# Optimization experiments

Measured on AMD Instinct MI355X. Metric: run time of the kernel, lower is better.

Reference implementation:

```python
import jax, jax.numpy as jnp
import numpy as np
from jax import lax

# config (matches init_kwargs)
NUM_CLASSES = 10
SCORE_THRESH = 0.05
TOPK = 1000
DET_PER_IMG = 100
NMS_SCORE = 0.3
NMS_SIGMA = 0.5
IMG_H, IMG_W = 800.0, 1333.0
IOU_SUPPRESS = 0.8
BBOX_XFORM_CLIP = float(np.log(1000.0 / 16.0))
EPS = 1e-7


def setup_inputs() -> dict:
    key = jax.random.key(0)
    k1, k2, k3 = jax.random.split(key, 3)
    B, A, C = 8, 200000, NUM_CLASSES
    cls_logits = jax.random.normal(k1, (B, A, C), dtype=jnp.float32)
    bbox_regression = 0.5 * jax.random.normal(k2, (B, A, 4), dtype=jnp.float32)
    # plausible anchors: random centers + sizes inside the image, xyxy format
    u = jax.random.uniform(k3, (A, 6), dtype=jnp.float32)
    cx = u[:, 0] * IMG_W
    cy = u[:, 1] * IMG_H
    w = 16.0 + u[:, 2] * 200.0
    h = 16.0 + u[:, 3] * 200.0
    anchors = jnp.stack([cx - 0.5 * w, cy - 0.5 * h, cx + 0.5 * w, cy + 0.5 * h], axis=-1)
    return {"cls_logits": cls_logits, "bbox_regression": bbox_regression, "anchors": anchors}


def _decode(rel, anc):
    # torchvision BoxCoder.decode_single, weights (1,1,1,1). rel, anc: [K,4] xyxy anchors
    wa = anc[:, 2] - anc[:, 0]
    ha = anc[:, 3] - anc[:, 1]
    cxa = anc[:, 0] + 0.5 * wa
    cya = anc[:, 1] + 0.5 * ha
    dx, dy = rel[:, 0], rel[:, 1]
    dw = jnp.minimum(rel[:, 2], BBOX_XFORM_CLIP)
    dh = jnp.minimum(rel[:, 3], BBOX_XFORM_CLIP)
    cx = dx * wa + cxa
    cy = dy * ha + cya
    w = jnp.exp(dw) * wa
    h = jnp.exp(dh) * ha
    boxes = jnp.stack([cx - 0.5 * w, cy - 0.5 * h, cx + 0.5 * w, cy + 0.5 * h], axis=-1)
    # clip_boxes_to_image
    x = jnp.clip(boxes[:, 0::2], 0.0, IMG_W)
    y = jnp.clip(boxes[:, 1::2], 0.0, IMG_H)
    return jnp.stack([x[:, 0], y[:, 0], x[:, 1], y[:, 1]], axis=-1)


def _iou_one(box, boxes):
    # box [4] vs boxes [K,4] -> [K]
    lt = jnp.maximum(box[:2], boxes[:, :2])
    rb = jnp.minimum(box[2:], boxes[:, 2:])
    wh = jnp.clip(rb - lt, 0.0)
    inter = wh[:, 0] * wh[:, 1]
    a1 = (box[2] - box[0]) * (box[3] - box[1])
    a2 = (boxes[:, 2] - boxes[:, 0]) * (boxes[:, 3] - boxes[:, 1])
    return inter / (a1 + a2 - inter + EPS)


def _postprocess_one(logits, rel, anchors):
    # logits [A,C], rel [A,4], anchors [A,4]
    probs = jax.nn.sigmoid(logits)
    scores_all = jnp.max(probs, axis=-1)               # [A]
    labels_all = jnp.argmax(probs, axis=-1)            # [A]
    scores_all = jnp.where(scores_all > SCORE_THRESH, scores_all, 0.0)
    top_scores, top_idx = lax.top_k(scores_all, TOPK)  # [K]
    labels = labels_all[top_idx]
    boxes = _decode(rel[top_idx], anchors[top_idx])    # [K,4]

    K = TOPK
    # --- batched gaussian soft-NMS (same-label decay only) ---
    def soft_step(carry, _):
        sc, out = carry
        i = jnp.argmax(sc)
        s = sc[i]
        out = out.at[i].set(jnp.maximum(s, 0.0))
        ious = _iou_one(boxes[i], boxes)
        decay = jnp.where(labels == labels[i], jnp.exp(-(ious ** 2) / NMS_SIGMA), 1.0)
        sc = (sc * decay).at[i].set(-1.0)
        return (sc, out), None
    (_, decayed), _ = lax.scan(soft_step, (top_scores, jnp.zeros_like(top_scores)), None, length=K)
    keep = decayed > NMS_SCORE

    # --- sort by decayed score desc, greedy hard suppression at IoU>0.8 ---
    order = jnp.argsort(-decayed)
    b = boxes[order]
    s = decayed[order]
    l = labels[order]
    alive0 = keep[order]
    idxs = jnp.arange(K)

    def greedy_step(alive, i):
        ious = _iou_one(b[i], b)
        suppress = (ious > IOU_SUPPRESS) & (idxs > i)
        alive = jnp.where(alive[i], alive & ~suppress, alive)
        return alive, None
    alive, _ = lax.scan(greedy_step, alive0, idxs)

    final_scores = jnp.where(alive, s, -1.0)
    out_scores, out_i = lax.top_k(final_scores, DET_PER_IMG)  # preserves desc order of survivors
    return b[out_i], out_scores, l[out_i]


def reference(cls_logits, bbox_regression, anchors):
    boxes, scores, labels = jax.vmap(_postprocess_one, in_axes=(0, 0, None))(
        cls_logits, bbox_regression, anchors)
    return boxes, scores, labels  # [B,D,4], [B,D], [B,D] (score -1 = padding)
```

## Files before the change

kernel.cpp:

```cpp
#include <hip/hip_runtime.h>
#include <math.h>

#define NCLS 10
#define TOPK 1000
#define DETS 100
#define CANDMAX 4096
#define SLOTS 16
#define ACTK 256
#define TILE 256

#define NB2 256
#define MGATE (-2.9444389791664403f)
#define SEAM 2.2f
#define SCA 30.907200f
#define SCB 41.0f
#define NBLK 64

__device__ __forceinline__ float sigmoidf_(float x) {
    return 1.0f / (1.0f + expf(-x));
}

__device__ __forceinline__ int mbin_(float m) {
    if (!(m > MGATE)) return 0;
    int b;
    if (m > SEAM) { b = 161 + (int)((m - SEAM) * SCB); if (b > 255) b = 255; }
    else          { b = 1 + (int)((m - MGATE) * SCA);  if (b > 160) b = 160; }
    return b;
}

__device__ __forceinline__ float key_score(const unsigned long long* key, int c) {
    return __uint_as_float(~(unsigned)(key[c] >> 32));
}

__device__ __forceinline__ unsigned fkey_(float f) {
    unsigned b = __float_as_uint(f);
    return (b & 0x80000000u) ? ~b : (b | 0x80000000u);
}
__device__ __forceinline__ float funkey_(unsigned k) {
    return __uint_as_float((k & 0x80000000u) ? (k & 0x7FFFFFFFu) : ~k);
}

__device__ __forceinline__ unsigned wave_umax_(unsigned x) {
    unsigned t;
    t = (unsigned)__builtin_amdgcn_update_dpp(0, (int)x, 0x111, 0xF, 0xF, false); x = (x > t) ? x : t;
    t = (unsigned)__builtin_amdgcn_update_dpp(0, (int)x, 0x112, 0xF, 0xF, false); x = (x > t) ? x : t;
    t = (unsigned)__builtin_amdgcn_update_dpp(0, (int)x, 0x114, 0xF, 0xF, false); x = (x > t) ? x : t;
    t = (unsigned)__builtin_amdgcn_update_dpp(0, (int)x, 0x118, 0xF, 0xF, false); x = (x > t) ? x : t;
    t = (unsigned)__builtin_amdgcn_update_dpp(0, (int)x, 0x142, 0xF, 0xF, false); x = (x > t) ? x : t;
    t = (unsigned)__builtin_amdgcn_update_dpp(0, (int)x, 0x143, 0xF, 0xF, false); x = (x > t) ? x : t;
    return (unsigned)__builtin_amdgcn_readlane((int)x, 63);
}

__global__ __launch_bounds__(256) void k_score_bins(const float* __restrict__ logits,
                                                    unsigned char* __restrict__ binc,
                                                    unsigned* hist,
                                                    unsigned* __restrict__ done,
                                                    unsigned* __restrict__ P,
                                                    int A) {
    __shared__ float tilef[TILE * NCLS];
    __shared__ unsigned h[4][NB2];
    __shared__ int s_last;
    int img = blockIdx.y;
    int tid = threadIdx.x;
    for (int i = tid; i < 4 * NB2; i += 256) ((unsigned*)h)[i] = 0;
    __syncthreads();

    const float* base = logits + (size_t)img * A * NCLS;
    unsigned char* bc = binc + (size_t)img * A;
    int rep = tid & 3;

    int ntile = A / TILE;
    for (int tile = blockIdx.x; tile < ntile; tile += NBLK) {
        const float4* src = (const float4*)(base + (size_t)tile * TILE * NCLS);
        float4 v0 = src[tid];
        float4 v1 = src[256 + tid];
        float4 v2;
        if (tid < 128) v2 = src[512 + tid];
        ((float4*)tilef)[tid] = v0;
        ((float4*)tilef)[256 + tid] = v1;
        if (tid < 128) ((float4*)tilef)[512 + tid] = v2;
        __syncthreads();
        float m = tilef[tid * 10];
#pragma unroll
        for (int c = 1; c < 10; ++c) m = fmaxf(m, tilef[tid * 10 + c]);
        int b = mbin_(m);
        bc[(size_t)tile * TILE + tid] = (unsigned char)b;
        if (b) atomicAdd(&h[rep][b], 1u);
        __syncthreads();
    }
    if (blockIdx.x == 0) {
        for (int a = ntile * TILE + tid; a < A; a += 256) {
            const float* lp2 = base + (size_t)a * NCLS;
            float m = lp2[0];
            for (int c = 1; c < 10; ++c) m = fmaxf(m, lp2[c]);
            int b = mbin_(m);
            bc[a] = (unsigned char)b;
            if (b) atomicAdd(&h[rep][b], 1u);
        }
    }
    __syncthreads();
    for (int i = tid; i < NB2; i += 256) {
        unsigned c = h[0][i] + h[1][i] + h[2][i] + h[3][i];
        if (c) atomicAdd(&hist[(size_t)img * NB2 + i], c);
    }
    __syncthreads();
    if (tid == 0) {
        __threadfence();
        unsigned old = atomicAdd(&done[img], 1u);
        s_last = (old == (unsigned)(NBLK - 1)) ? 1 : 0;
    }
    __syncthreads();
    if (s_last && tid < 64) {
        int lane = tid;
        unsigned* hh = hist + (size_t)img * NB2;
        unsigned b4[4];
        unsigned s = 0;
#pragma unroll
        for (int j = 0; j < 4; ++j) { b4[j] = atomicAdd(&hh[lane * 4 + j], 0u); s += b4[j]; }
        unsigned suf = s;
#pragma unroll
        for (int d = 1; d < 64; d <<= 1) {
            unsigned o = __shfl_down(suf, d);
            if (lane + d < 64) suf += o;
        }
        unsigned above = __shfl_down(suf, 1);
        if (lane == 63) above = 0;
        if (lane == 0 && suf < (unsigned)TOPK) P[img] = 0u;
        if (above < (unsigned)TOPK && suf >= (unsigned)TOPK) {
            unsigned cum = above;
            for (int j = 3; j >= 0; --j) {
                cum += b4[j];
                if (cum >= (unsigned)TOPK) { P[img] = (unsigned)(lane * 4 + j); break; }
            }
        }
    }
}

__global__ __launch_bounds__(256) void k_compact(const float* __restrict__ logits,
                                                 const unsigned char* __restrict__ binc,
                                                 const unsigned* __restrict__ P,
                                                 unsigned* __restrict__ ctr,
                                                 unsigned long long* __restrict__ cand,
                                                 int A) {
    int img = blockIdx.y;
    unsigned p = P[img];
    unsigned psel = p ? (p - 1u) : 0u;
    int lane = threadIdx.x & 63;
    const float* base = logits + (size_t)img * A * NCLS;
    const unsigned* b4 = (const unsigned*)(binc + (size_t)img * A);
    int nquad = A >> 2;
    for (int q = blockIdx.x * 256 + threadIdx.x; q < nquad; q += NBLK * 256) {
        unsigned ub = b4[q];
#pragma unroll
        for (int j = 0; j < 4; ++j) {
            unsigned bj = (ub >> (8 * j)) & 0xFFu;
            bool take = (psel == 0u) || (bj >= psel);
            unsigned long long mask = __ballot(take);
            if (mask) {
                int cnt = __popcll(mask);
                int leader = __ffsll((unsigned long long)mask) - 1;
                unsigned pos = 0;
                if (lane == leader) pos = atomicAdd(&ctr[img], (unsigned)cnt);
                pos = (unsigned)__shfl((int)pos, leader);
                if (take) {
                    unsigned slot = pos + (unsigned)__popcll(mask & ((1ull << lane) - 1ull));
                    if (slot < CANDMAX) {
                        unsigned a = (unsigned)(q * 4 + j);
                        const float* lp = base + (size_t)a * NCLS;
                        float m = lp[0];
#pragma unroll
                        for (int c = 1; c < 10; ++c) m = fmaxf(m, lp[c]);
                        float sc = sigmoidf_(m);
                        sc = (sc > 0.05f) ? sc : 0.0f;
                        unsigned bits = __float_as_uint(sc);
                        cand[(size_t)img * CANDMAX + slot] =
                            ((unsigned long long)bits << 32) | (unsigned)(~a);
                    }
                }
            }
        }
    }
    int tail0 = nquad << 2;
    if (blockIdx.x == 0) {
        for (int a = tail0 + (int)threadIdx.x; a < A; a += 256) {
            unsigned bj = binc[(size_t)img * A + a];
            if ((psel == 0u) || (bj >= psel)) {
                const float* lp = base + (size_t)a * NCLS;
                float m = lp[0];
                for (int c = 1; c < 10; ++c) m = fmaxf(m, lp[c]);
                float sc = sigmoidf_(m);
                sc = (sc > 0.05f) ? sc : 0.0f;
                unsigned bits = __float_as_uint(sc);
                unsigned pos = atomicAdd(&ctr[img], 1u);
                if (pos < CANDMAX)
                    cand[(size_t)img * CANDMAX + pos] =
                        ((unsigned long long)bits << 32) | (unsigned)(~a);
            }
        }
    }
}

__global__ __launch_bounds__(1024) void k_sortnms(const unsigned long long* __restrict__ cand,
                                                  const unsigned* __restrict__ ctr,
                                                  const float* __restrict__ logits,
                                                  const float* __restrict__ rel,
                                                  const float* __restrict__ anch,
                                                  float* __restrict__ out, int A, int B) {
    __shared__ unsigned long long key[CANDMAX];
    __shared__ float s_box[TOPK][4];
    __shared__ int   s_lab[TOPK];
    __shared__ float s_pbox[TOPK][4];
    __shared__ int   s_plab[TOPK];
    __shared__ float s_psc[TOPK];
    __shared__ int   s_alive[TOPK];

    const float CLIPV = 4.135166556742356f;
    const float EPS = 1e-7f;
    const float W_ = 1333.0f, H_ = 800.0f;

    int img = blockIdx.x;
    int tid = threadIdx.x;

    unsigned n = ctr[img];
    if (n > CANDMAX) n = CANDMAX;
    int L = (n <= 1024) ? 1024 : (n <= 2048) ? 2048 : CANDMAX;
    for (int i = tid; i < L; i += 1024)
        key[i] = (i < (int)n) ? ~cand[(size_t)img * CANDMAX + i] : ~0ull;
    __syncthreads();
    for (int k = 2; k <= L; k <<= 1) {
        for (int j = k >> 1; j > 0; j >>= 1) {
            for (int i = tid; i < L; i += 1024) {
                int l = i ^ j;
                if (l > i) {
                    unsigned long long va = key[i], vb = key[l];
                    bool up = ((i & k) == 0);
                    if (up ? (va > vb) : (va < vb)) { key[i] = vb; key[l] = va; }
                }
            }
            __syncthreads();
        }
    }
    for (int i = L + tid; i < CANDMAX; i += 1024) key[i] = ~0ull;
    __syncthreads();

    if (tid < TOPK) {
        unsigned long long ik = key[tid];
        unsigned ai = (unsigned)ik;
        if (ai >= (unsigned)A) ai = 0;
        const float* lp = logits + ((size_t)img * A + ai) * NCLS;
        float best = sigmoidf_(lp[0]); int lbb = 0;
#pragma unroll
        for (int cc = 1; cc < NCLS; ++cc) {
            float v = sigmoidf_(lp[cc]);
            if (v > best) { best = v; lbb = cc; }
        }
        const float* rp = rel + ((size_t)img * A + ai) * 4;
        const float* ap = anch + (size_t)ai * 4;
        float a0 = ap[0], a1 = ap[1], a2 = ap[2], a3 = ap[3];
        float wa = a2 - a0, ha = a3 - a1;
        float cxa = a0 + 0.5f * wa, cya = a1 + 0.5f * ha;
        float dx = rp[0], dy = rp[1];
        float dw = fminf(rp[2], CLIPV), dh = fminf(rp[3], CLIPV);
        float cx = dx * wa + cxa, cy = dy * ha + cya;
        float w = expf(dw) * wa, h = expf(dh) * ha;
        s_box[tid][0] = fminf(fmaxf(cx - 0.5f * w, 0.0f), W_);
        s_box[tid][1] = fminf(fmaxf(cy - 0.5f * h, 0.0f), H_);
        s_box[tid][2] = fminf(fmaxf(cx + 0.5f * w, 0.0f), W_);
        s_box[tid][3] = fminf(fmaxf(cy + 0.5f * h, 0.0f), H_);
        s_lab[tid] = lbb;
    }
    __syncthreads();
    if (tid >= 64) return;
    int lane = tid;

    int M = TOPK;
    int need_full = 0;
    float bound = key_score(key, ACTK);

    {
        float sc[4], x1[4], y1[4], x2[4], y2[4], ar[4];
        int lb[4];
#pragma unroll
        for (int j = 0; j < 4; ++j) {
            int c = lane + (j << 6);
            float4 bb = *(const float4*)&s_box[c][0];
            x1[j] = bb.x; y1[j] = bb.y; x2[j] = bb.z; y2[j] = bb.w;
            ar[j] = (bb.z - bb.x) * (bb.w - bb.y);
            lb[j] = s_lab[c];
            sc[j] = key_score(key, c);
        }

        int nconf = 0, Mf = -1;

        for (int t = 0; t < ACTK; ++t) {
            float bv = sc[0]; int bj = 0;
#pragma unroll
            for (int j = 1; j < 4; ++j)
                if (sc[j] > bv) { bv = sc[j]; bj = j; }
            unsigned mk = fkey_(bv);
            unsigned mx = wave_umax_(mk);
            float pcur = funkey_(mx);

            if (!(pcur >= bound)) { need_full = 1; break; }

            int pick = -1;
#pragma unroll
            for (int jj = 0; jj < 4; ++jj) {
                if (pick < 0) {
                    unsigned long long mj = __ballot(mk == mx && bj == jj);
                    if (mj) pick = (jj << 6) + (__ffsll(mj) - 1);
                }
            }

            float psc = fmaxf(pcur, 0.0f);
            float4 pb = *(const float4*)&s_box[pick][0];
            int plab_ = s_lab[pick];
            if (lane == 0) {
                *(float4*)&s_pbox[t][0] = pb;
                s_plab[t] = plab_;
                s_psc[t] = psc;
            }

            float4 qb[4]; int ga[4];
#pragma unroll
            for (int k = 0; k < 4; ++k) {
                int p = lane + (k << 6);
                int pc2 = (p < t) ? p : 0;
                qb[k] = *(const float4*)&s_pbox[pc2][0];
                ga[k] = (p < t) ? s_alive[pc2] : 0;
            }

            float wax = (pb.z - pb.x) * (pb.w - pb.y);
#pragma unroll
            for (int j = 0; j < 4; ++j) {
                float lx2 = fmaxf(pb.x, x1[j]), ly2 = fmaxf(pb.y, y1[j]);
                float rx2 = fminf(pb.z, x2[j]), ry2 = fminf(pb.w, y2[j]);
                float iw2 = fmaxf(rx2 - lx2, 0.0f), ih2 = fmaxf(ry2 - ly2, 0.0f);
                float inter2 = iw2 * ih2;
                bool hot = (inter2 > 0.0f) && (lb[j] == plab_);
                if (__ballot(hot) != 0ull) {
                    float iou2 = inter2 / (wax + ar[j] - inter2 + EPS);
                    float ie = (lb[j] == plab_) ? iou2 : 0.0f;
                    sc[j] *= expf(-(ie * ie) / 0.5f);
                }
            }
#pragma unroll
            for (int j = 0; j < 4; ++j)
                if (lane + (j << 6) == pick) sc[j] = -1.0f;

            bool sup = false;
#pragma unroll
            for (int k = 0; k < 4; ++k) {
                if (ga[k]) {
                    float lx = fmaxf(pb.x, qb[k].x), ly = fmaxf(pb.y, qb[k].y);
                    float rx = fminf(pb.z, qb[k].z), ry = fminf(pb.w, qb[k].w);
                    float iw = fmaxf(rx - lx, 0.0f), ih = fmaxf(ry - ly, 0.0f);
                    float inter = iw * ih;
                    float qa = (qb[k].z - qb[k].x) * (qb[k].w - qb[k].y);
                    float iou = inter / (wax + qa - inter + EPS);
                    sup = sup || (iou > 0.8f);
                }
            }
            bool alive = (psc > 0.3f) && (__ballot(sup) == 0ull);
            if (lane == 0) s_alive[t] = alive ? 1 : 0;
            nconf += alive ? 1 : 0;
            if (nconf >= DETS) { Mf = t + 1; break; }
        }
        if (!need_full) {
            if (Mf < 0) need_full = 1;
            else M = Mf;
        }
    }

    if (need_full) {
        float sc[SLOTS], x1[SLOTS], y1[SLOTS], x2[SLOTS], y2[SLOTS], ar[SLOTS];
        int lb[SLOTS];
#pragma unroll
        for (int j = 0; j < SLOTS; ++j) {
            int c = lane + (j << 6);
            if (c < TOPK) {
                float4 bb = *(const float4*)&s_box[c][0];
                x1[j] = bb.x; y1[j] = bb.y; x2[j] = bb.z; y2[j] = bb.w;
                ar[j] = (bb.z - bb.x) * (bb.w - bb.y);
                lb[j] = s_lab[c];
                sc[j] = key_score(key, c);
            } else {
                sc[j] = -2.0f; lb[j] = -1;
                x1[j] = y1[j] = x2[j] = y2[j] = ar[j] = 0.0f;
            }
        }
        unsigned long long aw = 0;
        if (lane < 15) aw = ~0ull;
        else if (lane == 15) aw = (1ull << (TOPK - 15 * 64)) - 1;
        int f = 0, nconf = 0;
        M = TOPK;
        for (int t = 0; t < TOPK; ++t) {
            int fp = (f < TOPK) ? f : 0;
            float4 fb = *(const float4*)&s_box[fp][0];
            int flab = s_lab[fp];
            int fs = f >> 6;
            float v = sc[0];
#pragma unroll
            for (int j = 1; j < SLOTS; ++j) if (fs == j) v = sc[j];
            float cf = __shfl(v, f & 63);
            float lm = sc[0];
#pragma unroll
            for (int j = 1; j < SLOTS; ++j) lm = fmaxf(lm, sc[j]);
            int pick; float pcur; float4 pb; int plab_;
            unsigned long long bb2 = __ballot(lm > cf);
            if (bb2 == 0) {
                pick = f; pcur = cf; pb = fb; plab_ = flab;
            } else {
                float bv = sc[0]; int bi = lane;
#pragma unroll
                for (int j = 1; j < SLOTS; ++j) {
                    int e = lane + (j << 6);
                    if (sc[j] > bv) { bv = sc[j]; bi = e; }
                }
#pragma unroll
                for (int d = 32; d; d >>= 1) {
                    float ov = __shfl_xor(bv, d);
                    int oi = __shfl_xor(bi, d);
                    if (ov > bv || (ov == bv && oi < bi)) { bv = ov; bi = oi; }
                }
                pick = bi; pcur = bv;
                pb = *(const float4*)&s_box[pick][0];
                plab_ = s_lab[pick];
            }
            float psc = fmaxf(pcur, 0.0f);
            if (lane == 0) {
                *(float4*)&s_pbox[t][0] = pb;
                s_plab[t] = plab_;
                s_psc[t] = psc;
            }
            bool alive = (psc > 0.3f);
            if (alive && t > 0) {
                float pa = (pb.z - pb.x) * (pb.w - pb.y);
                int kprev = ((t - 1) >> 6) + 1;
                bool sup = false;
                for (int k = 0; k < kprev; ++k) {
                    int p = lane + (k << 6);
                    int pc = (p < t) ? p : 0;
                    float4 qb = *(const float4*)&s_pbox[pc][0];
                    int ga = s_alive[pc];
                    if (p < t && ga) {
                        float lx = fmaxf(pb.x, qb.x), ly = fmaxf(pb.y, qb.y);
                        float rx = fminf(pb.z, qb.z), ry = fminf(pb.w, qb.w);
                        float iw = fmaxf(rx - lx, 0.0f), ih = fmaxf(ry - ly, 0.0f);
                        float inter = iw * ih;
                        float qa = (qb.z - qb.x) * (qb.w - qb.y);
                        float iou = inter / (pa + qa - inter + EPS);
                        sup = sup || (iou > 0.8f);
                    }
                }
                alive = (__ballot(sup) == 0ull);
            }
            if (lane == 0) s_alive[t] = alive ? 1 : 0;
            nconf += alive ? 1 : 0;
            if (nconf >= DETS) { M = t + 1; break; }
            float wax = (pb.z - pb.x) * (pb.w - pb.y);
#pragma unroll
            for (int j = 0; j < SLOTS; ++j) {
                float lx2 = fmaxf(pb.x, x1[j]), ly2 = fmaxf(pb.y, y1[j]);
                float rx2 = fminf(pb.z, x2[j]), ry2 = fminf(pb.w, y2[j]);
                float iw2 = fmaxf(rx2 - lx2, 0.0f), ih2 = fmaxf(ry2 - ly2, 0.0f);
                float inter2 = iw2 * ih2;
                bool hot = (inter2 > 0.0f) && (lb[j] == plab_);
                if (__ballot(hot) != 0ull) {
                    float iou2 = inter2 / (wax + ar[j] - inter2 + EPS);
                    float ie = (lb[j] == plab_) ? iou2 : 0.0f;
                    sc[j] *= expf(-(ie * ie) / 0.5f);
                }
            }
#pragma unroll
            for (int j = 0; j < SLOTS; ++j)
                if (lane + (j << 6) == pick) sc[j] = -1.0f;
            if (lane == (pick >> 6)) aw &= ~(1ull << (pick & 63));
            if (pick == f) {
                int fw = f >> 6;
                unsigned long long w2 = __shfl(aw, fw);
                while (w2 == 0ull && fw < 15) { ++fw; w2 = __shfl(aw, fw); }
                f = (w2 == 0ull) ? TOPK : (fw << 6) + (__ffsll(w2) - 1);
            }
        }
    }

    float* out_boxes  = out;
    float* out_scores = out + (size_t)B * DETS * 4;
    float* out_labels = out + (size_t)B * DETS * 5;
    int kmax = (M + 63) >> 6;
    int base = 0;
    for (int k = 0; k < kmax; ++k) {
        int p = lane + (k << 6);
        bool av = (p < M) && (s_alive[p] != 0);
        unsigned long long mask = __ballot(av);
        int slot = base + (int)__popcll(mask & ((1ull << lane) - 1ull));
        if (av && slot < DETS) {
            float4 pb = *(const float4*)&s_pbox[p][0];
            float* ob = out_boxes + ((size_t)img * DETS + slot) * 4;
            ob[0] = pb.x; ob[1] = pb.y; ob[2] = pb.z; ob[3] = pb.w;
            out_scores[img * DETS + slot] = s_psc[p];
            out_labels[img * DETS + slot] = (float)s_plab[p];
        }
        base += (int)__popcll(mask);
    }
    if (base < DETS) {
        int dbase = 0;
        for (int k = 0; k < kmax; ++k) {
            int p = lane + (k << 6);
            bool dd = (p < M) && (s_alive[p] == 0);
            unsigned long long mask = __ballot(dd);
            int slot = base + dbase + (int)__popcll(mask & ((1ull << lane) - 1ull));
            if (dd && slot < DETS) {
                float4 pb = *(const float4*)&s_pbox[p][0];
                float* ob = out_boxes + ((size_t)img * DETS + slot) * 4;
                ob[0] = pb.x; ob[1] = pb.y; ob[2] = pb.z; ob[3] = pb.w;
                out_scores[img * DETS + slot] = -1.0f;
                out_labels[img * DETS + slot] = (float)s_plab[p];
            }
            dbase += (int)__popcll(mask);
        }
    }
}

extern "C" void kernel_launch(void* const* d_in, const int* in_sizes, int n_in,
                              void* d_out, int out_size, void* d_ws, size_t ws_size,
                              hipStream_t stream) {
    const float* logits = (const float*)d_in[0];
    const float* rel = (const float*)d_in[1];
    const float* anch = (const float*)d_in[2];
    float* out = (float*)d_out;

    int A = in_sizes[2] / 4;
    int B = in_sizes[0] / (A * NCLS);

    char* w = (char*)d_ws;
    unsigned* hist = (unsigned*)w;           w += (size_t)B * NB2 * 4;
    unsigned* ctr = (unsigned*)w;            w += (size_t)B * 4;
    unsigned* done = (unsigned*)w;           w += (size_t)B * 4;
    size_t zbytes = (size_t)(w - (char*)d_ws);
    unsigned long long* cand = (unsigned long long*)w; w += (size_t)B * CANDMAX * 8;
    unsigned* P = (unsigned*)w;              w += (size_t)B * 4;
    unsigned char* binc = (unsigned char*)w;

    hipMemsetAsync(d_ws, 0, zbytes, stream);

    dim3 g1(NBLK, (unsigned)B);
    k_score_bins<<<g1, 256, 0, stream>>>(logits, binc, hist, done, P, A);
    k_compact<<<g1, 256, 0, stream>>>(logits, binc, P, ctr, cand, A);
    k_sortnms<<<B, 1024, 0, stream>>>(cand, ctr, logits, rel, anch, out, A, B);
}
```

Measured before the change: 258.1 us.

## Fuse candidate compaction into sort kernel and widen histogram grid

```diff
diff --git a/kernel.cpp b/kernel.cpp
--- a/kernel.cpp
+++ b/kernel.cpp
@@ -14,7 +14,7 @@
 #define SEAM 2.2f
 #define SCA 30.907200f
 #define SCB 41.0f
-#define NBLK 64
+#define NBLKB 256
 
 __device__ __forceinline__ float sigmoidf_(float x) {
     return 1.0f / (1.0f + expf(-x));
@@ -70,7 +70,7 @@
     int rep = tid & 3;
 
     int ntile = A / TILE;
-    for (int tile = blockIdx.x; tile < ntile; tile += NBLK) {
+    for (int tile = blockIdx.x; tile < ntile; tile += NBLKB) {
         const float4* src = (const float4*)(base + (size_t)tile * TILE * NCLS);
         float4 v0 = src[tid];
         float4 v1 = src[256 + tid];
@@ -107,7 +107,7 @@
     if (tid == 0) {
         __threadfence();
         unsigned old = atomicAdd(&done[img], 1u);
-        s_last = (old == (unsigned)(NBLK - 1)) ? 1 : 0;
+        s_last = (old == (unsigned)(NBLKB - 1)) ? 1 : 0;
     }
     __syncthreads();
     if (s_last && tid < 64) {
@@ -136,72 +136,8 @@
     }
 }
 
-__global__ __launch_bounds__(256) void k_compact(const float* __restrict__ logits,
-                                                 const unsigned char* __restrict__ binc,
-                                                 const unsigned* __restrict__ P,
-                                                 unsigned* __restrict__ ctr,
-                                                 unsigned long long* __restrict__ cand,
-                                                 int A) {
-    int img = blockIdx.y;
-    unsigned p = P[img];
-    unsigned psel = p ? (p - 1u) : 0u;
-    int lane = threadIdx.x & 63;
-    const float* base = logits + (size_t)img * A * NCLS;
-    const unsigned* b4 = (const unsigned*)(binc + (size_t)img * A);
-    int nquad = A >> 2;
-    for (int q = blockIdx.x * 256 + threadIdx.x; q < nquad; q += NBLK * 256) {
-        unsigned ub = b4[q];
-#pragma unroll
-        for (int j = 0; j < 4; ++j) {
-            unsigned bj = (ub >> (8 * j)) & 0xFFu;
-            bool take = (psel == 0u) || (bj >= psel);
-            unsigned long long mask = __ballot(take);
-            if (mask) {
-                int cnt = __popcll(mask);
-                int leader = __ffsll((unsigned long long)mask) - 1;
-                unsigned pos = 0;
-                if (lane == leader) pos = atomicAdd(&ctr[img], (unsigned)cnt);
-                pos = (unsigned)__shfl((int)pos, leader);
-                if (take) {
-                    unsigned slot = pos + (unsigned)__popcll(mask & ((1ull << lane) - 1ull));
-                    if (slot < CANDMAX) {
-                        unsigned a = (unsigned)(q * 4 + j);
-                        const float* lp = base + (size_t)a * NCLS;
-                        float m = lp[0];
-#pragma unroll
-                        for (int c = 1; c < 10; ++c) m = fmaxf(m, lp[c]);
-                        float sc = sigmoidf_(m);
-                        sc = (sc > 0.05f) ? sc : 0.0f;
-                        unsigned bits = __float_as_uint(sc);
-                        cand[(size_t)img * CANDMAX + slot] =
-                            ((unsigned long long)bits << 32) | (unsigned)(~a);
-                    }
-                }
-            }
-        }
-    }
-    int tail0 = nquad << 2;
-    if (blockIdx.x == 0) {
-        for (int a = tail0 + (int)threadIdx.x; a < A; a += 256) {
-            unsigned bj = binc[(size_t)img * A + a];
-            if ((psel == 0u) || (bj >= psel)) {
-                const float* lp = base + (size_t)a * NCLS;
-                float m = lp[0];
-                for (int c = 1; c < 10; ++c) m = fmaxf(m, lp[c]);
-                float sc = sigmoidf_(m);
-                sc = (sc > 0.05f) ? sc : 0.0f;
-                unsigned bits = __float_as_uint(sc);
-                unsigned pos = atomicAdd(&ctr[img], 1u);
-                if (pos < CANDMAX)
-                    cand[(size_t)img * CANDMAX + pos] =
-                        ((unsigned long long)bits << 32) | (unsigned)(~a);
-            }
-        }
-    }
-}
-
-__global__ __launch_bounds__(1024) void k_sortnms(const unsigned long long* __restrict__ cand,
-                                                  const unsigned* __restrict__ ctr,
+__global__ __launch_bounds__(1024) void k_sortnms(const unsigned char* __restrict__ binc,
+                                                  const unsigned* __restrict__ P,
                                                   const float* __restrict__ logits,
                                                   const float* __restrict__ rel,
                                                   const float* __restrict__ anch,
@@ -213,6 +149,7 @@
     __shared__ int   s_plab[TOPK];
     __shared__ float s_psc[TOPK];
     __shared__ int   s_alive[TOPK];
+    __shared__ unsigned s_n;
 
     const float CLIPV = 4.135166556742356f;
     const float EPS = 1e-7f;
@@ -220,13 +157,73 @@
 
     int img = blockIdx.x;
     int tid = threadIdx.x;
-
-    unsigned n = ctr[img];
+    const float* base = logits + (size_t)img * A * NCLS;
+
+    if (tid == 0) s_n = 0;
+    __syncthreads();
+    {
+        unsigned p = P[img];
+        unsigned psel = p ? (p - 1u) : 0u;
+        const unsigned* b4 = (const unsigned*)(binc + (size_t)img * A);
+        int nquad = A >> 2;
+        int nq4 = nquad >> 2;
+        for (int g = tid; g < nq4; g += 1024) {
+            uint4 u = ((const uint4*)b4)[g];
+            unsigned ws[4] = {u.x, u.y, u.z, u.w};
+#pragma unroll
+            for (int w2 = 0; w2 < 4; ++w2) {
+                unsigned ub = ws[w2];
+#pragma unroll
+                for (int j = 0; j < 4; ++j) {
+                    unsigned bj = (ub >> (8 * j)) & 0xFFu;
+                    if ((psel == 0u) || (bj >= psel)) {
+                        unsigned pos = atomicAdd(&s_n, 1u);
+                        if (pos < CANDMAX)
+                            key[pos] = (unsigned long long)(unsigned)((g * 4 + w2) * 4 + j);
+                    }
+                }
+            }
+        }
+        for (int q = (nq4 << 2) + tid; q < nquad; q += 1024) {
+            unsigned ub = b4[q];
+#pragma unroll
+            for (int j = 0; j < 4; ++j) {
+                unsigned bj = (ub >> (8 * j)) & 0xFFu;
+                if ((psel == 0u) || (bj >= psel)) {
+                    unsigned pos = atomicAdd(&s_n, 1u);
+                    if (pos < CANDMAX)
+                        key[pos] = (unsigned long long)(unsigned)(q * 4 + j);
+                }
+            }
+        }
+        for (int a = (nquad << 2) + tid; a < A; a += 1024) {
+            unsigned bj = binc[(size_t)img * A + a];
+            if ((psel == 0u) || (bj >= psel)) {
+                unsigned pos = atomicAdd(&s_n, 1u);
+                if (pos < CANDMAX)
+                    key[pos] = (unsigned long long)(unsigned)a;
+            }
+        }
+    }
+    __syncthreads();
+    unsigned n = s_n;
     if (n > CANDMAX) n = CANDMAX;
     int L = (n <= 1024) ? 1024 : (n <= 2048) ? 2048 : CANDMAX;
-    for (int i = tid; i < L; i += 1024)
-        key[i] = (i < (int)n) ? ~cand[(size_t)img * CANDMAX + i] : ~0ull;
-    __syncthreads();
+
+    for (int t2 = tid; t2 < (int)n; t2 += 1024) {
+        unsigned a = (unsigned)key[t2];
+        const float* lp = base + (size_t)a * NCLS;
+        float m = lp[0];
+#pragma unroll
+        for (int c = 1; c < 10; ++c) m = fmaxf(m, lp[c]);
+        float sc = sigmoidf_(m);
+        sc = (sc > 0.05f) ? sc : 0.0f;
+        unsigned bits = __float_as_uint(sc);
+        key[t2] = ((unsigned long long)(~bits) << 32) | a;
+    }
+    for (int i = (int)n + tid; i < CANDMAX; i += 1024) key[i] = ~0ull;
+    __syncthreads();
+
     for (int k = 2; k <= L; k <<= 1) {
         for (int j = k >> 1; j > 0; j >>= 1) {
             for (int i = tid; i < L; i += 1024) {
@@ -240,14 +237,12 @@
             __syncthreads();
         }
     }
-    for (int i = L + tid; i < CANDMAX; i += 1024) key[i] = ~0ull;
-    __syncthreads();
 
     if (tid < TOPK) {
         unsigned long long ik = key[tid];
         unsigned ai = (unsigned)ik;
         if (ai >= (unsigned)A) ai = 0;
-        const float* lp = logits + ((size_t)img * A + ai) * NCLS;
+        const float* lp = base + (size_t)ai * NCLS;
         float best = sigmoidf_(lp[0]); int lbb = 0;
 #pragma unroll
         for (int cc = 1; cc < NCLS; ++cc) {
@@ -489,12 +484,12 @@
     float* out_scores = out + (size_t)B * DETS * 4;
     float* out_labels = out + (size_t)B * DETS * 5;
     int kmax = (M + 63) >> 6;
-    int base = 0;
+    int base2 = 0;
     for (int k = 0; k < kmax; ++k) {
         int p = lane + (k << 6);
         bool av = (p < M) && (s_alive[p] != 0);
         unsigned long long mask = __ballot(av);
-        int slot = base + (int)__popcll(mask & ((1ull << lane) - 1ull));
+        int slot = base2 + (int)__popcll(mask & ((1ull << lane) - 1ull));
         if (av && slot < DETS) {
             float4 pb = *(const float4*)&s_pbox[p][0];
             float* ob = out_boxes + ((size_t)img * DETS + slot) * 4;
@@ -502,15 +497,15 @@
             out_scores[img * DETS + slot] = s_psc[p];
             out_labels[img * DETS + slot] = (float)s_plab[p];
         }
-        base += (int)__popcll(mask);
-    }
-    if (base < DETS) {
+        base2 += (int)__popcll(mask);
+    }
+    if (base2 < DETS) {
         int dbase = 0;
         for (int k = 0; k < kmax; ++k) {
             int p = lane + (k << 6);
             bool dd = (p < M) && (s_alive[p] == 0);
             unsigned long long mask = __ballot(dd);
-            int slot = base + dbase + (int)__popcll(mask & ((1ull << lane) - 1ull));
+            int slot = base2 + dbase + (int)__popcll(mask & ((1ull << lane) - 1ull));
             if (dd && slot < DETS) {
                 float4 pb = *(const float4*)&s_pbox[p][0];
                 float* ob = out_boxes + ((size_t)img * DETS + slot) * 4;
@@ -536,17 +531,14 @@
 
     char* w = (char*)d_ws;
     unsigned* hist = (unsigned*)w;           w += (size_t)B * NB2 * 4;
-    unsigned* ctr = (unsigned*)w;            w += (size_t)B * 4;
     unsigned* done = (unsigned*)w;           w += (size_t)B * 4;
     size_t zbytes = (size_t)(w - (char*)d_ws);
-    unsigned long long* cand = (unsigned long long*)w; w += (size_t)B * CANDMAX * 8;
     unsigned* P = (unsigned*)w;              w += (size_t)B * 4;
     unsigned char* binc = (unsigned char*)w;
 
     hipMemsetAsync(d_ws, 0, zbytes, stream);
 
-    dim3 g1(NBLK, (unsigned)B);
+    dim3 g1(NBLKB, (unsigned)B);
     k_score_bins<<<g1, 256, 0, stream>>>(logits, binc, hist, done, P, A);
-    k_compact<<<g1, 256, 0, stream>>>(logits, binc, P, ctr, cand, A);
-    k_sortnms<<<B, 1024, 0, stream>>>(cand, ctr, logits, rel, anch, out, A, B);
-}
+    k_sortnms<<<B, 1024, 0, stream>>>(binc, P, logits, rel, anch, out, A, B);
+}
```

Result: faster. 226.6 us, median of 2 (-12.2%).
